# Kernel optimization log

Measured on AMD Instinct MI355X. Metric: run time of the kernel, lower is better.

Reference implementation:

```python
import jax, jax.numpy as jnp
import numpy as np

B, T, D = 32, 2048, 256
K, NC = 1024, 8  # codebook_size, n_codebooks


def setup_inputs() -> dict:
    key = jax.random.key(0)
    k1, k2 = jax.random.split(key)
    z = jax.random.normal(k1, (B, T, D), dtype=jnp.float32)
    # nn.init.uniform_(weight, -1/codebook_size, 1/codebook_size)
    codebooks = jax.random.uniform(k2, (NC, K, D), dtype=jnp.float32,
                                   minval=-1.0 / K, maxval=1.0 / K)
    return {"z": z, "codebooks": codebooks}


def _rvq(z, codebooks):
    """Residual VQ: sequential nearest-codeword quantization over NC codebooks."""
    def step(carry, W):  # W: [K, D]
        residual, quantized, loss = carry
        flat = residual.reshape(-1, W.shape[-1])  # [N, D]
        # Squared L2 distances; argmin identical to torch.cdist(p=2).argmin
        d2 = (jnp.sum(flat * flat, axis=-1, keepdims=True)
              - 2.0 * (flat @ W.T)
              + jnp.sum(W * W, axis=-1))  # [N, K]
        idx = jnp.argmin(d2, axis=-1)  # [N] int
        q_i = W[idx].reshape(residual.shape)  # embedding lookup
        new_res = residual - q_i
        # F.mse_loss(residual_after, zeros) = mean(residual_after**2)
        loss = loss + jnp.mean(new_res * new_res)
        return (new_res, quantized + q_i, loss), idx

    init = (z, jnp.zeros_like(z), jnp.float32(0.0))
    (_, quantized, commitment_loss), idxs = jax.lax.scan(step, init, codebooks)
    indices_stack = idxs.T  # [N, NC], matches torch.stack(indices_list, dim=-1)
    return quantized, indices_stack, commitment_loss


def reference(z, codebooks):
    return _rvq(z, codebooks)
```

## Files before the change

### kernel.cpp

```cpp
#include <hip/hip_runtime.h>

#define NROWS 65536
#define DD 256
#define KK 1024
#define NCB 8
#define QN 16777216
#define IDXN 524288
#define MARGIN 4e-3f
#define ROWS 64
#define QCAP 1024

typedef __attribute__((ext_vector_type(8))) short bf16x8;
typedef __attribute__((ext_vector_type(4))) float f32x4;
typedef unsigned long long u64;

__device__ __forceinline__ float fp32_barrier(float x) {
    asm volatile("" : "+v"(x));
    return x;
}

__device__ __forceinline__ unsigned short f2bf(float x) {
    union { float f; unsigned u; } v; v.f = x;
    return (unsigned short)((v.u + 0x7fffu + ((v.u >> 16) & 1u)) >> 16);
}

__device__ __forceinline__ u64 enc_sc(float sc, int k) {
    unsigned u = __float_as_uint(sc);
    u = ((int)u < 0) ? ~u : (u | 0x80000000u);
    return ((u64)u << 32) | (unsigned)k;
}

__device__ __forceinline__ float dec_sc(u64 e) {
    unsigned u = (unsigned)(e >> 32);
    u = (u & 0x80000000u) ? (u & 0x7fffffffu) : ~u;
    return __uint_as_float(u);
}

typedef const __attribute__((address_space(1))) void* gas_ptr;
typedef __attribute__((address_space(3))) void* las_ptr;
__device__ __forceinline__ void gll16(const float* g, float* l) {
    __builtin_amdgcn_global_load_lds((gas_ptr)g, (las_ptr)l, 16, 0, 0);
}

__global__ void wss_kernel(const float* __restrict__ cb, float* __restrict__ wss) {
    const int g = blockIdx.x * blockDim.x + threadIdx.x;
    if (g >= NCB * KK) return;
    const float* w = cb + (size_t)g * DD;
    float res0 = 0.f, res1 = 0.f;
    #pragma unroll
    for (int half = 0; half < 2; ++half) {
        const float* p = w + half * 128;
        float acc[8];
        #pragma unroll
        for (int j = 0; j < 8; ++j) acc[j] = fp32_barrier(p[j] * p[j]);
        #pragma unroll
        for (int i = 8; i < 128; i += 8)
            #pragma unroll
            for (int j = 0; j < 8; ++j) acc[j] += fp32_barrier(p[i + j] * p[i + j]);
        const float t = ((acc[0] + acc[1]) + (acc[2] + acc[3])) +
                        ((acc[4] + acc[5]) + (acc[6] + acc[7]));
        if (half == 0) res0 = t; else res1 = t;
    }
    wss[g] = res0 + res1;
}

__global__ void wbf_kernel(const float* __restrict__ cb, uint4* __restrict__ Wbf) {
    const int g = blockIdx.x * 256 + threadIdx.x;
    const int klocal = g & 63;
    const int kgt = (g >> 6) & 31;
    const int kg = kgt & 3;
    const int t  = kgt >> 2;
    const int ch = (g >> 11) & 15;
    const int c  = g >> 15;
    const float* src = cb + (size_t)(c * 1024 + ch * 64 + klocal) * DD + t * 32 + kg * 8;
    const float4 v0 = *(const float4*)(src);
    const float4 v1 = *(const float4*)(src + 4);
    uint4 o;
    o.x = (unsigned)f2bf(v0.x) | ((unsigned)f2bf(v0.y) << 16);
    o.y = (unsigned)f2bf(v0.z) | ((unsigned)f2bf(v0.w) << 16);
    o.z = (unsigned)f2bf(v1.x) | ((unsigned)f2bf(v1.y) << 16);
    o.w = (unsigned)f2bf(v1.z) | ((unsigned)f2bf(v1.w) << 16);
    Wbf[g] = o;
}

__global__ void probe_kernel(float* __restrict__ flagp) {
    const int l = threadIdx.x;
    const int m = l & 15, kb = (l >> 4) * 8;
    bf16x8 a1, a2, b1, b2;
    #pragma unroll
    for (int e = 0; e < 8; ++e) {
        a1[e] = (short)f2bf((float)m);
        a2[e] = (short)f2bf((float)(kb + e));
        b1[e] = (short)f2bf((kb + e == 5) ? 1.f : 0.f);
        b2[e] = (short)f2bf((kb + e == 5 && m == 3) ? 1.f : 0.f);
    }
    f32x4 z = {0.f, 0.f, 0.f, 0.f};
    f32x4 d1 = __builtin_amdgcn_mfma_f32_16x16x32_bf16(a1, b1, z, 0, 0, 0);
    f32x4 d2 = __builtin_amdgcn_mfma_f32_16x16x32_bf16(a2, b2, z, 0, 0, 0);
    bool ok = true;
    const int col = l & 15, rbase = (l >> 4) * 4;
    #pragma unroll
    for (int reg = 0; reg < 4; ++reg) {
        ok = ok && (d1[reg] == (float)(rbase + reg));
        ok = ok && (d2[reg] == ((col == 3) ? 5.f : 0.f));
    }
    const int good = __all(ok ? 1 : 0);
    if (l == 0) *flagp = good ? 3.0f : 1.0f;
}

__launch_bounds__(512, 1)
__global__ void step_all_kernel(const float* __restrict__ z, const float* __restrict__ cb,
                                const unsigned short* __restrict__ Wbf,
                                float* __restrict__ out_idx, const float* __restrict__ wss,
                                double* __restrict__ loss, const float* __restrict__ flagp,
                                float* __restrict__ outq)
{
    __shared__ float r_s[ROWS][260];
    __shared__ __align__(16) char pool[65536];
    __shared__ float wss_s[KK];
    __shared__ float rss_s[ROWS];
    __shared__ float rminp[ROWS][2];
    __shared__ float rmin_s[ROWS];
    __shared__ unsigned qbuf[QCAP];
    __shared__ u64 encmin[ROWS];
    __shared__ int rowbad[ROWS];
    __shared__ int ovfq[ROWS];
    __shared__ int novf, qn;
    __shared__ int hist_s[ROWS][NCB];
    __shared__ double lred[8];
    __shared__ u64 warena[8];

    const int tid = threadIdx.x;
    const int lane = tid & 63;
    const int wv = tid >> 6;
    const int row0 = blockIdx.x * ROWS;
    const int row = tid >> 3;
    const int d0 = (tid & 7) * 32;

    {
        const float* zr = z + (size_t)(row0 + row) * DD + d0;
        #pragma unroll
        for (int q = 0; q < 8; ++q)
            *(float4*)&r_s[row][d0 + q * 4] = *(const float4*)(zr + q * 4);
    }
    const int flag = (int)*flagp;

    unsigned short (*rb)[264] = (unsigned short(*)[264])pool;

    #pragma unroll 1
    for (int c = 0; c < NCB; ++c) {
        const size_t cK = (size_t)c * KK;
        if (tid < ROWS) { rowbad[tid] = 0; encmin[tid] = 0xFFFFFFFFFFFFFFFFULL; }
        if (tid == 0) { novf = 0; qn = 0; }
        qbuf[tid] = 0xFFFFFFFFu;
        qbuf[tid + 512] = 0xFFFFFFFFu;
        __syncthreads();

        {
            unsigned* rbrow = (unsigned*)&rb[row][0];
            #pragma unroll
            for (int j = 0; j < 16; ++j) {
                const float a = r_s[row][d0 + 2 * j];
                const float b = r_s[row][d0 + 2 * j + 1];
                rbrow[d0 / 2 + j] = (unsigned)f2bf(a) | ((unsigned)f2bf(b) << 16);
            }
        }
        if (tid < ROWS) {
            float res[2];
            #pragma unroll
            for (int half = 0; half < 2; ++half) {
                const int base = half * 128;
                float acc[8];
                #pragma unroll
                for (int j = 0; j < 8; ++j) {
                    const float x = r_s[tid][base + j];
                    acc[j] = fp32_barrier(x * x);
                }
                #pragma unroll
                for (int i = 8; i < 128; i += 8)
                    #pragma unroll
                    for (int j = 0; j < 8; ++j) {
                        const float x = r_s[tid][base + i + j];
                        acc[j] += fp32_barrier(x * x);
                    }
                res[half] = ((acc[0] + acc[1]) + (acc[2] + acc[3])) +
                            ((acc[4] + acc[5]) + (acc[6] + acc[7]));
            }
            rss_s[tid] = res[0] + res[1];
        }

        if (flag == 3) {
            const int rg = wv & 3;
            const int kh = wv >> 2;
            const int mrow0 = rg * 16;
            const int colk = lane & 15, kg = lane >> 4;
            const int lanebase = kg * 512 + kh * 256 + colk * 8;

            __syncthreads();
            bf16x8 af[8];
            #pragma unroll
            for (int t = 0; t < 8; ++t)
                af[t] = *(const bf16x8*)&rb[mrow0 + colk][t * 32 + kg * 8];

            float rssA[4];
            u64 best1[4], best2[4];
            #pragma unroll
            for (int reg = 0; reg < 4; ++reg) {
                rssA[reg] = rss_s[mrow0 + kg * 4 + reg];
                best1[reg] = 0xFFFFFFFFFFFFFFFFULL;
                best2[reg] = 0xFFFFFFFFFFFFFFFFULL;
            }
            wss_s[tid] = wss[cK + tid];
            wss_s[tid + 512] = wss[cK + tid + 512];
            __syncthreads();

            unsigned short* buf0 = (unsigned short*)pool;
            unsigned short* buf1 = (unsigned short*)(pool + 32768);
            const unsigned short* WbfC = Wbf + cK * 256;

            {
                const float* src = (const float*)WbfC;
                #pragma unroll
                for (int q = 0; q < 4; ++q) {
                    const int f = tid + 512 * q;
                    gll16(src + f * 4, (float*)buf0 + f * 4);
                }
            }
            __syncthreads();

            #pragma unroll 1
            for (int ch = 0; ch < 16; ++ch) {
                unsigned short* cur = (ch & 1) ? buf1 : buf0;
                unsigned short* nxt = (ch & 1) ? buf0 : buf1;
                if (ch + 1 < 16) {
                    const float* src = (const float*)(WbfC + (size_t)(ch + 1) * 16384);
                    #pragma unroll
                    for (int q = 0; q < 4; ++q) {
                        const int f = tid + 512 * q;
                        gll16(src + f * 4, (float*)nxt + f * 4);
                    }
                }
                #pragma unroll
                for (int s16 = 0; s16 < 2; ++s16) {
                    f32x4 acc = {0.f, 0.f, 0.f, 0.f};
                    #pragma unroll
                    for (int t = 0; t < 8; ++t) {
                        const bf16x8 bfv = *(const bf16x8*)
                            &cur[t * 2048 + s16 * 128 + lanebase];
                        acc = __builtin_amdgcn_mfma_f32_16x16x32_bf16(af[t], bfv, acc, 0, 0, 0);
                    }
                    const int k = ch * 64 + kh * 32 + s16 * 16 + colk;
                    const float ws = wss_s[k];
                    #pragma unroll
                    for (int reg = 0; reg < 4; ++reg) {
                        const float sA = __builtin_fmaf(-2.f, acc[reg], rssA[reg]) + ws;
                        const u64 e = enc_sc(sA, k);
                        const bool lt1 = e < best1[reg];
                        const u64 m2cand = (e < best2[reg]) ? e : best2[reg];
                        best2[reg] = lt1 ? best1[reg] : m2cand;
                        best1[reg] = lt1 ? e : best1[reg];
                    }
                }
                __syncthreads();
            }

            #pragma unroll
            for (int reg = 0; reg < 4; ++reg) {
                u64 rm = best1[reg];
                #pragma unroll
                for (int off = 1; off < 16; off <<= 1) {
                    const u64 o = __shfl_xor(rm, off);
                    if (o < rm) rm = o;
                }
                if (colk == 0) rminp[mrow0 + kg * 4 + reg][kh] = dec_sc(rm);
            }
            __syncthreads();
            if (tid < ROWS) rmin_s[tid] = fminf(rminp[tid][0], rminp[tid][1]);
            __syncthreads();

            #pragma unroll
            for (int reg = 0; reg < 4; ++reg) {
                const int rrow = mrow0 + kg * 4 + reg;
                const float th = rmin_s[rrow] + MARGIN;
                unsigned tu = __float_as_uint(th);
                tu = ((int)tu < 0) ? ~tu : (tu | 0x80000000u);
                const u64 th_enc = ((u64)tu << 32) | 0xFFFFFFFFULL;
                if (best1[reg] <= th_enc) {
                    if (best2[reg] <= th_enc) {
                        const int base = atomicAdd(&qn, 32);
                        if (base + 32 <= QCAP) {
                            int p = base;
                            #pragma unroll
                            for (int c2 = 0; c2 < 16; ++c2)
                                #pragma unroll
                                for (int s2 = 0; s2 < 2; ++s2)
                                    qbuf[p++] = ((unsigned)rrow << 10) |
                                        (unsigned)(c2 * 64 + kh * 32 + s2 * 16 + colk);
                        } else rowbad[rrow] = 1;
                    } else {
                        const int base = atomicAdd(&qn, 1);
                        if (base < QCAP)
                            qbuf[base] = ((unsigned)rrow << 10) |
                                         (unsigned)(best1[reg] & 1023ULL);
                        else rowbad[rrow] = 1;
                    }
                }
            }
            __syncthreads();

            {
                const int nq = (qn < QCAP) ? qn : QCAP;
                for (int i = tid; i < nq; i += 512) {
                    const unsigned it = qbuf[i];
                    if (it == 0xFFFFFFFFu) continue;
                    const int rrow = it >> 10, k = (int)(it & 1023u);
                    const float* wr = cb + (cK + k) * DD;
                    float a = 0.f;
                    for (int q = 0; q < 64; ++q) {
                        const float4 w4 = *(const float4*)(wr + q * 4);
                        a = __builtin_fmaf(r_s[rrow][q * 4 + 0], w4.x, a);
                        a = __builtin_fmaf(r_s[rrow][q * 4 + 1], w4.y, a);
                        a = __builtin_fmaf(r_s[rrow][q * 4 + 2], w4.z, a);
                        a = __builtin_fmaf(r_s[rrow][q * 4 + 3], w4.w, a);
                    }
                    const float sc = (rss_s[rrow] - 2.0f * a) + wss_s[k];
                    atomicMin(&encmin[rrow], enc_sc(sc, k));
                }
            }
            __syncthreads();
            if (tid < ROWS) {
                if (rowbad[tid] || encmin[tid] == 0xFFFFFFFFFFFFFFFFULL) {
                    ovfq[atomicAdd(&novf, 1)] = tid;
                } else {
                    const int ki = (int)(encmin[tid] & 0xFFFFFFFFULL);
                    out_idx[(size_t)(row0 + tid) * NCB + c] = (float)ki;
                    hist_s[tid][c] = ki;
                }
            }
            __syncthreads();
            const int nqo = novf;
            for (int qi = 0; qi < nqo; ++qi) {
                const int orow = ovfq[qi];
                const float rs = rss_s[orow];
                u64 best = 0xFFFFFFFFFFFFFFFFULL;
                for (int k = tid; k < KK; k += 512) {
                    const float* wr = cb + (cK + k) * DD;
                    float a = 0.f;
                    for (int q = 0; q < 64; ++q) {
                        const float4 w4 = *(const float4*)(wr + q * 4);
                        a = __builtin_fmaf(r_s[orow][q * 4 + 0], w4.x, a);
                        a = __builtin_fmaf(r_s[orow][q * 4 + 1], w4.y, a);
                        a = __builtin_fmaf(r_s[orow][q * 4 + 2], w4.z, a);
                        a = __builtin_fmaf(r_s[orow][q * 4 + 3], w4.w, a);
                    }
                    const u64 e = enc_sc((rs - 2.0f * a) + wss[cK + k], k);
                    if (e < best) best = e;
                }
                #pragma unroll
                for (int off = 1; off < 64; off <<= 1) {
                    const u64 o = __shfl_xor(best, off);
                    if (o < best) best = o;
                }
                if (lane == 0) warena[wv] = best;
                __syncthreads();
                if (tid == 0) {
                    u64 m = warena[0];
                    #pragma unroll
                    for (int w = 1; w < 8; ++w) if (warena[w] < m) m = warena[w];
                    const int ki = (int)(m & 0xFFFFFFFFULL);
                    out_idx[(size_t)(row0 + orow) * NCB + c] = (float)ki;
                    hist_s[orow][c] = ki;
                }
                __syncthreads();
            }
        } else {
            __syncthreads();
            u64* fb_s = (u64*)qbuf;
            {
                const int frow = tid >> 3, band = tid & 7;
                const float frss = rss_s[frow];
                u64 fb = 0xFFFFFFFFFFFFFFFFULL;
                const float* cbc = cb + cK * DD;
                for (int k = band * 128; k < band * 128 + 128; ++k) {
                    const float* wr = cbc + (size_t)k * DD;
                    float a = 0.f;
                    for (int q = 0; q < 64; ++q) {
                        const float4 w4 = *(const float4*)(wr + q * 4);
                        a = __builtin_fmaf(r_s[frow][q * 4 + 0], w4.x, a);
                        a = __builtin_fmaf(r_s[frow][q * 4 + 1], w4.y, a);
                        a = __builtin_fmaf(r_s[frow][q * 4 + 2], w4.z, a);
                        a = __builtin_fmaf(r_s[frow][q * 4 + 3], w4.w, a);
                    }
                    const u64 e = enc_sc((frss - 2.0f * a) + wss[cK + k], k);
                    if (e < fb) fb = e;
                }
                fb_s[frow * 8 + band] = fb;
            }
            __syncthreads();
            if (tid < ROWS) {
                u64 m = fb_s[tid * 8];
                #pragma unroll
                for (int j = 1; j < 8; ++j) if (fb_s[tid * 8 + j] < m) m = fb_s[tid * 8 + j];
                const int ki = (int)(m & 0xFFFFFFFFULL);
                out_idx[(size_t)(row0 + tid) * NCB + c] = (float)ki;
                hist_s[tid][c] = ki;
            }
        }
        __syncthreads();

        {
            const int k = hist_s[row][c];
            const float* w = cb + (cK + (size_t)k) * DD + d0;
            double ssq = 0.0;
            #pragma unroll
            for (int q = 0; q < 8; ++q) {
                const float4 wv4 = *(const float4*)(w + q * 4);
                float4 rv = *(float4*)&r_s[row][d0 + q * 4];
                rv.x -= wv4.x; rv.y -= wv4.y; rv.z -= wv4.z; rv.w -= wv4.w;
                *(float4*)&r_s[row][d0 + q * 4] = rv;
                ssq += (double)rv.x * rv.x; ssq += (double)rv.y * rv.y;
                ssq += (double)rv.z * rv.z; ssq += (double)rv.w * rv.w;
            }
            for (int off = 32; off; off >>= 1) ssq += __shfl_down(ssq, off);
            if (lane == 0) lred[wv] = ssq;
        }
        __syncthreads();
        if (tid == 0) {
            double s = 0.0;
            #pragma unroll
            for (int w = 0; w < 8; ++w) s += lred[w];
            atomicAdd(&loss[c], s);
        }
    }
    __syncthreads();

    {
        float qa[32];
        #pragma unroll
        for (int j = 0; j < 32; ++j) qa[j] = 0.f;
        for (int j = 0; j < NCB; ++j) {
            const int k = hist_s[row][j];
            const float* w = cb + ((size_t)j * KK + k) * DD + d0;
            #pragma unroll
            for (int q = 0; q < 8; ++q) {
                const float4 wv4 = *(const float4*)(w + q * 4);
                qa[q * 4 + 0] += wv4.x; qa[q * 4 + 1] += wv4.y;
                qa[q * 4 + 2] += wv4.z; qa[q * 4 + 3] += wv4.w;
            }
        }
        float* dst = outq + (size_t)(row0 + row) * DD + d0;
        #pragma unroll
        for (int q = 0; q < 8; ++q)
            *(float4*)(dst + q * 4) =
                make_float4(qa[q * 4], qa[q * 4 + 1], qa[q * 4 + 2], qa[q * 4 + 3]);
    }
}

__global__ void loss_write_kernel(const double* __restrict__ loss,
                                  float* __restrict__ out_loss) {
    double s = 0.0;
    for (int i = 0; i < NCB; ++i) s += loss[i];
    *out_loss = (float)(s / 16777216.0);
}

extern "C" void kernel_launch(void* const* d_in, const int* in_sizes, int n_in,
                              void* d_out, int out_size, void* d_ws, size_t ws_size,
                              hipStream_t stream)
{
    const float* z  = (const float*)d_in[0];
    const float* cb = (const float*)d_in[1];
    float* outq     = (float*)d_out;
    float* out_idx  = outq + QN;
    float* out_loss = outq + QN + IDXN;

    double* loss  = (double*)d_ws;
    float*  flagp = (float*)((char*)d_ws + 576);
    float*  wss   = (float*)((char*)d_ws + 1024);
    unsigned short* Wbf = (unsigned short*)((char*)d_ws + 65536);

    hipMemsetAsync(d_ws, 0, 1024, stream);
    probe_kernel<<<dim3(1), dim3(64), 0, stream>>>(flagp);
    wss_kernel<<<dim3((NCB * KK + 255) / 256), dim3(256), 0, stream>>>(cb, wss);
    wbf_kernel<<<dim3(1024), dim3(256), 0, stream>>>(cb, (uint4*)Wbf);
    step_all_kernel<<<dim3(NROWS / ROWS), dim3(512), 0, stream>>>(
        z, cb, Wbf, out_idx, wss, loss, flagp, outq);
    loss_write_kernel<<<1, 1, 0, stream>>>(loss, out_loss);
}
```

Measured before the change: 1.831 ms.

## Triple-buffer codebook chunks with prefetch depth two and vmcnt-based waits

Splits each codebook into 32 chunks of 32 codewords instead of 16 of 64, and cycles three 16KB LDS buffers so two chunks are in flight while one is consumed. The full __syncthreads is replaced by explicit s_waitcnt vmcnt plus s_barrier, so the wait covers only the older outstanding loads. The bf16 repack kernel layout and the candidate-enumeration indexing are updated to the new chunk shape. LDS use drops from 64KB to 48KB, but there are twice as many barriers and less MFMA work per chunk. The hand-set vmcnt counts must match the real number of outstanding loads, or buffers could be read before they arrive.

```diff
diff --git a/kernel.cpp b/kernel.cpp
--- a/kernel.cpp
+++ b/kernel.cpp
@@ -9,6 +9,7 @@
 #define MARGIN 4e-3f
 #define ROWS 64
 #define QCAP 1024
+#define NCH 32
 
 typedef __attribute__((ext_vector_type(8))) short bf16x8;
 typedef __attribute__((ext_vector_type(4))) float f32x4;
@@ -66,13 +67,12 @@
 
 __global__ void wbf_kernel(const float* __restrict__ cb, uint4* __restrict__ Wbf) {
     const int g = blockIdx.x * 256 + threadIdx.x;
-    const int klocal = g & 63;
-    const int kgt = (g >> 6) & 31;
-    const int kg = kgt & 3;
-    const int t  = kgt >> 2;
-    const int ch = (g >> 11) & 15;
+    const int klocal = g & 31;
+    const int kg = (g >> 5) & 3;
+    const int t  = (g >> 7) & 7;
+    const int ch = (g >> 10) & 31;
     const int c  = g >> 15;
-    const float* src = cb + (size_t)(c * 1024 + ch * 64 + klocal) * DD + t * 32 + kg * 8;
+    const float* src = cb + (size_t)(c * 1024 + ch * 32 + klocal) * DD + t * 32 + kg * 8;
     const float4 v0 = *(const float4*)(src);
     const float4 v1 = *(const float4*)(src + 4);
     uint4 o;
@@ -116,7 +116,7 @@
                                 float* __restrict__ outq)
 {
     __shared__ float r_s[ROWS][260];
-    __shared__ __align__(16) char pool[65536];
+    __shared__ __align__(16) char pool[49152];
     __shared__ float wss_s[KK];
     __shared__ float rss_s[ROWS];
     __shared__ float rminp[ROWS][2];
@@ -194,7 +194,7 @@
             const int kh = wv >> 2;
             const int mrow0 = rg * 16;
             const int colk = lane & 15, kg = lane >> 4;
-            const int lanebase = kg * 512 + kh * 256 + colk * 8;
+            const int lanebase = kg * 256 + kh * 128 + colk * 8;
 
             __syncthreads();
             bf16x8 af[8];
@@ -214,42 +214,42 @@
             wss_s[tid + 512] = wss[cK + tid + 512];
             __syncthreads();
 
-            unsigned short* buf0 = (unsigned short*)pool;
-            unsigned short* buf1 = (unsigned short*)(pool + 32768);
             const unsigned short* WbfC = Wbf + cK * 256;
 
-            {
-                const float* src = (const float*)WbfC;
-                #pragma unroll
-                for (int q = 0; q < 4; ++q) {
+            #pragma unroll
+            for (int pc = 0; pc < 2; ++pc) {
+                const float* src = (const float*)(WbfC + (size_t)pc * 8192);
+                float* lb = (float*)(pool + 16384 * pc);
+                #pragma unroll
+                for (int q = 0; q < 2; ++q) {
                     const int f = tid + 512 * q;
-                    gll16(src + f * 4, (float*)buf0 + f * 4);
-                }
-            }
-            __syncthreads();
+                    gll16(src + f * 4, lb + f * 4);
+                }
+            }
+            asm volatile("s_waitcnt vmcnt(2)" ::: "memory");
+            __builtin_amdgcn_sched_barrier(0);
+            __builtin_amdgcn_s_barrier();
 
             #pragma unroll 1
-            for (int ch = 0; ch < 16; ++ch) {
-                unsigned short* cur = (ch & 1) ? buf1 : buf0;
-                unsigned short* nxt = (ch & 1) ? buf0 : buf1;
-                if (ch + 1 < 16) {
-                    const float* src = (const float*)(WbfC + (size_t)(ch + 1) * 16384);
+            for (int ch = 0; ch < NCH; ++ch) {
+                if (ch + 2 < NCH) {
+                    const float* src = (const float*)(WbfC + (size_t)(ch + 2) * 8192);
+                    float* lb = (float*)(pool + 16384 * ((ch + 2) % 3));
                     #pragma unroll
-                    for (int q = 0; q < 4; ++q) {
+                    for (int q = 0; q < 2; ++q) {
                         const int f = tid + 512 * q;
-                        gll16(src + f * 4, (float*)nxt + f * 4);
-                    }
-                }
-                #pragma unroll
-                for (int s16 = 0; s16 < 2; ++s16) {
+                        gll16(src + f * 4, lb + f * 4);
+                    }
+                }
+                const unsigned short* cur = (const unsigned short*)(pool + 16384 * (ch % 3));
+                {
                     f32x4 acc = {0.f, 0.f, 0.f, 0.f};
                     #pragma unroll
                     for (int t = 0; t < 8; ++t) {
-                        const bf16x8 bfv = *(const bf16x8*)
-                            &cur[t * 2048 + s16 * 128 + lanebase];
+                        const bf16x8 bfv = *(const bf16x8*)&cur[t * 1024 + lanebase];
                         acc = __builtin_amdgcn_mfma_f32_16x16x32_bf16(af[t], bfv, acc, 0, 0, 0);
                     }
-                    const int k = ch * 64 + kh * 32 + s16 * 16 + colk;
+                    const int k = ch * 32 + kh * 16 + colk;
                     const float ws = wss_s[k];
                     #pragma unroll
                     for (int reg = 0; reg < 4; ++reg) {
@@ -261,7 +261,13 @@
                         best1[reg] = lt1 ? e : best1[reg];
                     }
                 }
-                __syncthreads();
+                if (ch < NCH - 2) {
+                    asm volatile("s_waitcnt vmcnt(2)" ::: "memory");
+                } else {
+                    asm volatile("s_waitcnt vmcnt(0)" ::: "memory");
+                }
+                __builtin_amdgcn_sched_barrier(0);
+                __builtin_amdgcn_s_barrier();
             }
 
             #pragma unroll
@@ -291,11 +297,9 @@
                         if (base + 32 <= QCAP) {
                             int p = base;
                             #pragma unroll
-                            for (int c2 = 0; c2 < 16; ++c2)
-                                #pragma unroll
-                                for (int s2 = 0; s2 < 2; ++s2)
-                                    qbuf[p++] = ((unsigned)rrow << 10) |
-                                        (unsigned)(c2 * 64 + kh * 32 + s2 * 16 + colk);
+                            for (int c2 = 0; c2 < 32; ++c2)
+                                qbuf[p++] = ((unsigned)rrow << 10) |
+                                    (unsigned)(c2 * 32 + kh * 16 + colk);
                         } else rowbad[rrow] = 1;
                     } else {
                         const int base = atomicAdd(&qn, 1);
```

Measured after the change: 1.962 ms. 7.2% more time.
